# Optimization experiments

Hardware: AMD Instinct MI355X
Metric: run time of the kernel (lower is better)

The kernel has to match this reference:

```python
import jax, jax.numpy as jnp
import numpy as np

ALPHA = 6.0
BETA = 1.8
D = 256
P = 4096


def setup_inputs() -> dict:
    key = jax.random.key(0)
    k1, k2, k3 = jax.random.split(key, 3)
    pts = jax.random.normal(k1, (1, 16384, 3), dtype=jnp.float32)
    # strict_standard_normal is a shuffled Gaussian quantile grid; a standard
    # normal draw is statistically equivalent for a correctness baseline.
    A = jax.random.normal(k2, (3, D), dtype=jnp.float32) * ALPHA
    B = jax.random.normal(k3, (3, P), dtype=jnp.float32) * BETA
    return {"pts": pts, "A": A, "B": B}


def reference(pts, A, B):
    d = A.shape[-1]
    sqrt_d = jnp.asarray(d, jnp.float32) ** 0.5
    pA = pts @ A            # (b, n, d)
    pB = pts @ B            # (b, n, p)
    eA = jnp.concatenate([jnp.cos(pA), jnp.sin(pA)], axis=-1)  # (b, n, 2d)
    eB = jnp.concatenate([jnp.cos(pB), jnp.sin(pB)], axis=-1)  # (b, n, 2p)
    # linear-attention-style chain: eB @ (eB^T @ eA)
    T = jnp.einsum('bnp,bnd->bpd', eB, eA)   # (b, 2p, 2d)
    G = jnp.einsum('bnp,bpd->bnd', eB, T)    # (b, n, 2d)
    Gc = jax.lax.complex(G[..., :d], G[..., d:]) / jax.lax.complex(eA[..., :d], eA[..., d:])
    Gc = Gc / jnp.linalg.norm(Gc, axis=-1, keepdims=True) * sqrt_d
    return Gc
```

## Files before the change

kernel.cpp:

```cpp
#include <hip/hip_runtime.h>

#define NPTS 16384
#define DH 256
#define PH 4096
#define D2 512
#define LDA 40

typedef _Float16 f16;
typedef _Float16 f16x4 __attribute__((ext_vector_type(4)));
typedef _Float16 f16x8 __attribute__((ext_vector_type(8)));
typedef float f32x4 __attribute__((ext_vector_type(4)));

__device__ f16   g_eAt[D2][NPTS];
__device__ f16   g_Tt[8][D2][2*PH];
__device__ f16   g_Ts[D2][2*PH];
__device__ float g_G[4][NPTS][D2];

__device__ __forceinline__ void gload16(const void* g, void* l) {
    __builtin_amdgcn_global_load_lds((const __attribute__((address_space(1))) void*)g,
                                     (__attribute__((address_space(3))) void*)l, 16, 0, 0);
}

__global__ __launch_bounds__(256) void ker_pre(const float* __restrict__ pts,
                                               const float* __restrict__ A) {
    const int dd = blockIdx.x;
    const int t  = threadIdx.x;
    const float a0 = A[dd], a1 = A[DH + dd], a2 = A[2*DH + dd];
    f16* rowc = &g_eAt[dd][t*64];
    f16* rows = &g_eAt[DH + dd][t*64];
    #pragma unroll
    for (int s = 0; s < 8; ++s) {
        const int nb = t*64 + 8*s;
        f16x8 vc, vs;
        #pragma unroll
        for (int i = 0; i < 8; ++i) {
            const float* pr = pts + (size_t)(nb + i)*3;
            float sn, cs_; __sincosf(pr[0]*a0 + pr[1]*a1 + pr[2]*a2, &sn, &cs_);
            vc[i] = (f16)cs_; vs[i] = (f16)sn;
        }
        *(f16x8*)(rowc + 8*s) = vc;
        *(f16x8*)(rows + 8*s) = vs;
    }
}

__global__ __launch_bounds__(512) void ker_T(const float* __restrict__ pts,
                                             const float* __restrict__ B) {
    const int q0 = blockIdx.x * 64;
    const int d0 = blockIdx.y * 256;
    const int ks = blockIdx.z;
    const int t  = threadIdx.x;
    const int lane = t & 63, wid = t >> 6;
    const int wm = wid >> 2, wn = wid & 3;

    __shared__ f16 Al[128][LDA];
    __shared__ f16 Bl[256][32];

    f32x4 acc[4][4];
    #pragma unroll
    for (int a = 0; a < 4; ++a)
        #pragma unroll
        for (int bq = 0; bq < 4; ++bq) acc[a][bq] = (f32x4){0.f,0.f,0.f,0.f};

    const int qq  = t >> 3;
    const int nn0 = (t & 7) * 4;
    const float b0 = B[q0+qq], b1 = B[PH+q0+qq], b2 = B[2*PH+q0+qq];
    const int brow = 32*wid + (lane >> 2);
    const size_t bsrc0 = (size_t)(d0 + brow)*NPTS + 8*(lane & 3);
    const int mrow = wm*64 + (lane & 15);
    const int ncol = wn*64 + (lane & 15);
    const int kof  = (lane >> 4) * 8;

    for (int c = 0; c < 64; ++c) {
        const int nb = ks*2048 + c*32;
        __syncthreads();
        {
            const float* pbase = pts + (size_t)(nb + nn0)*3;
            const float4 P0 = *(const float4*)(pbase);
            const float4 P1 = *(const float4*)(pbase + 4);
            const float4 P2 = *(const float4*)(pbase + 8);
            const float px[4] = {P0.x, P0.w, P1.z, P2.y};
            const float py[4] = {P0.y, P1.x, P1.w, P2.z};
            const float pz[4] = {P0.z, P1.y, P2.x, P2.w};
            f16x4 vc, vs;
            #pragma unroll
            for (int u = 0; u < 4; ++u) {
                float sn, cc; __sincosf(px[u]*b0 + py[u]*b1 + pz[u]*b2, &sn, &cc);
                vc[u] = (f16)cc; vs[u] = (f16)sn;
            }
            *(f16x4*)&Al[qq][nn0]      = vc;
            *(f16x4*)&Al[64 + qq][nn0] = vs;
        }
        gload16(&g_eAt[0][0] + bsrc0 + (size_t)nb,                    &Bl[32*wid][0]);
        gload16(&g_eAt[0][0] + bsrc0 + (size_t)16*NPTS + (size_t)nb,  &Bl[32*wid + 16][0]);
        __syncthreads();
        f16x8 af[4], bf[4];
        #pragma unroll
        for (int mf = 0; mf < 4; ++mf) af[mf] = *(const f16x8*)&Al[mrow + mf*16][kof];
        #pragma unroll
        for (int nf = 0; nf < 4; ++nf) bf[nf] = *(const f16x8*)&Bl[ncol + nf*16][kof];
        #pragma unroll
        for (int mf = 0; mf < 4; ++mf)
            #pragma unroll
            for (int nf = 0; nf < 4; ++nf)
                acc[mf][nf] = __builtin_amdgcn_mfma_f32_16x16x32_f16(
                    af[mf], bf[nf], acc[mf][nf], 0, 0, 0);
    }
    #pragma unroll
    for (int mf = 0; mf < 4; ++mf) {
        const int qrow = q0 + mf*16 + (lane >> 4)*4;
        #pragma unroll
        for (int nf = 0; nf < 4; ++nf) {
            const int d = d0 + wn*64 + nf*16 + (lane & 15);
            f16x4 v;
            #pragma unroll
            for (int j = 0; j < 4; ++j) v[j] = (f16)acc[mf][nf][j];
            *(f16x4*)&g_Tt[ks][d][(size_t)wm*PH + qrow] = v;
        }
    }
}

__global__ __launch_bounds__(256) void ker_tsum() {
    const size_t i = ((size_t)blockIdx.x*256 + threadIdx.x) * 8;
    float o[8] = {0,0,0,0,0,0,0,0};
    #pragma unroll
    for (int z = 0; z < 8; ++z) {
        const f16x8 v = *(const f16x8*)(&g_Tt[z][0][0] + i);
        #pragma unroll
        for (int j = 0; j < 8; ++j) o[j] += (float)v[j];
    }
    f16x8 r;
    #pragma unroll
    for (int j = 0; j < 8; ++j) r[j] = (f16)o[j];
    *(f16x8*)(&g_Ts[0][0] + i) = r;
}

__global__ __launch_bounds__(512) void ker_G(const float* __restrict__ pts,
                                             const float* __restrict__ B) {
    const int n0 = blockIdx.x * 128;
    const int d0 = blockIdx.y * 256;
    const int ks = blockIdx.z;
    const int t  = threadIdx.x;
    const int lane = t & 63, wid = t >> 6;
    const int wm = wid >> 2, wn = wid & 3;

    __shared__ f16 Ac[128][LDA], As[128][LDA];
    __shared__ f16 Bc[256][32],  Bs[256][32];

    f32x4 acc[4][4];
    #pragma unroll
    for (int a = 0; a < 4; ++a)
        #pragma unroll
        for (int bq = 0; bq < 4; ++bq) acc[a][bq] = (f32x4){0.f,0.f,0.f,0.f};

    const int nn  = t >> 2;
    const int qq0 = (t & 3) * 8;
    const float px = pts[(size_t)(n0+nn)*3];
    const float py = pts[(size_t)(n0+nn)*3 + 1];
    const float pz = pts[(size_t)(n0+nn)*3 + 2];
    const int brow = 32*wid + (lane >> 2);
    const size_t bsrc0 = (size_t)(d0 + brow)*(2*PH) + 8*(lane & 3);
    const int mrow = wm*64 + (lane & 15);
    const int ncol = wn*64 + (lane & 15);
    const int kof  = (lane >> 4) * 8;

    for (int c = 0; c < 32; ++c) {
        const int qk = ks*1024 + c*32;
        __syncthreads();
        {
            const int qg = qk + qq0;
            const float4 bx0 = *(const float4*)&B[qg];
            const float4 bx1 = *(const float4*)&B[qg + 4];
            const float4 by0 = *(const float4*)&B[PH + qg];
            const float4 by1 = *(const float4*)&B[PH + qg + 4];
            const float4 bz0 = *(const float4*)&B[2*PH + qg];
            const float4 bz1 = *(const float4*)&B[2*PH + qg + 4];
            const float bx[8] = {bx0.x,bx0.y,bx0.z,bx0.w, bx1.x,bx1.y,bx1.z,bx1.w};
            const float by[8] = {by0.x,by0.y,by0.z,by0.w, by1.x,by1.y,by1.z,by1.w};
            const float bz[8] = {bz0.x,bz0.y,bz0.z,bz0.w, bz1.x,bz1.y,bz1.z,bz1.w};
            f16x8 vc, vs;
            #pragma unroll
            for (int u = 0; u < 8; ++u) {
                float sn, cc; __sincosf(px*bx[u] + py*by[u] + pz*bz[u], &sn, &cc);
                vc[u] = (f16)cc; vs[u] = (f16)sn;
            }
            *(f16x8*)&Ac[nn][qq0] = vc;
            *(f16x8*)&As[nn][qq0] = vs;
        }
        gload16(&g_Ts[0][0] + bsrc0 + (size_t)qk,                         &Bc[32*wid][0]);
        gload16(&g_Ts[0][0] + bsrc0 + (size_t)16*(2*PH) + (size_t)qk,     &Bc[32*wid + 16][0]);
        gload16(&g_Ts[0][0] + bsrc0 + (size_t)PH + (size_t)qk,            &Bs[32*wid][0]);
        gload16(&g_Ts[0][0] + bsrc0 + (size_t)(16*(2*PH) + PH) + (size_t)qk, &Bs[32*wid + 16][0]);
        __syncthreads();
        f16x8 a1[4], a2[4], b1[4], b2[4];
        #pragma unroll
        for (int mf = 0; mf < 4; ++mf) {
            a1[mf] = *(const f16x8*)&Ac[mrow + mf*16][kof];
            a2[mf] = *(const f16x8*)&As[mrow + mf*16][kof];
        }
        #pragma unroll
        for (int nf = 0; nf < 4; ++nf) {
            b1[nf] = *(const f16x8*)&Bc[ncol + nf*16][kof];
            b2[nf] = *(const f16x8*)&Bs[ncol + nf*16][kof];
        }
        #pragma unroll
        for (int mf = 0; mf < 4; ++mf)
            #pragma unroll
            for (int nf = 0; nf < 4; ++nf) {
                acc[mf][nf] = __builtin_amdgcn_mfma_f32_16x16x32_f16(
                    a1[mf], b1[nf], acc[mf][nf], 0, 0, 0);
                acc[mf][nf] = __builtin_amdgcn_mfma_f32_16x16x32_f16(
                    a2[mf], b2[nf], acc[mf][nf], 0, 0, 0);
            }
    }
    #pragma unroll
    for (int mf = 0; mf < 4; ++mf) {
        const int nbase = n0 + wm*64 + mf*16 + (lane >> 4)*4;
        #pragma unroll
        for (int nf = 0; nf < 4; ++nf) {
            const int d = d0 + wn*64 + nf*16 + (lane & 15);
            #pragma unroll
            for (int j = 0; j < 4; ++j)
                g_G[ks][nbase + j][d] = acc[mf][nf][j];
        }
    }
}

__global__ __launch_bounds__(256) void ker_fin(const float* __restrict__ pts,
                                               const float* __restrict__ A,
                                               float* __restrict__ out) {
    const int n = blockIdx.x;
    const int k = threadIdx.x;
    const float p0 = pts[(size_t)n*3], p1 = pts[(size_t)n*3+1], p2 = pts[(size_t)n*3+2];
    const float alp = p0*A[k] + p1*A[DH + k] + p2*A[2*DH + k];
    float sa, ca; __sincosf(alp, &sa, &ca);
    const float Gr = g_G[0][n][k]      + g_G[1][n][k]      + g_G[2][n][k]      + g_G[3][n][k];
    const float Gi = g_G[0][n][DH + k] + g_G[1][n][DH + k] + g_G[2][n][DH + k] + g_G[3][n][DH + k];
    const float Re = Gr*ca + Gi*sa;
    float nr = Gr*Gr + Gi*Gi;
    #pragma unroll
    for (int off = 32; off > 0; off >>= 1) nr += __shfl_down(nr, off, 64);
    __shared__ float wsum[4];
    if ((k & 63) == 0) wsum[k >> 6] = nr;
    __syncthreads();
    const float total = wsum[0] + wsum[1] + wsum[2] + wsum[3];
    const float scale = 16.0f * rsqrtf(total);
    out[(size_t)n*DH + k] = Re * scale;
}

extern "C" void kernel_launch(void* const* d_in, const int* in_sizes, int n_in,
                              void* d_out, int out_size, void* d_ws, size_t ws_size,
                              hipStream_t stream) {
    const float* pts = (const float*)d_in[0];
    const float* A   = (const float*)d_in[1];
    const float* B   = (const float*)d_in[2];
    float* out = (float*)d_out;
    (void)d_ws; (void)ws_size; (void)out_size;

    ker_pre <<<256, 256, 0, stream>>>(pts, A);
    ker_T   <<<dim3(64, 2, 8), 512, 0, stream>>>(pts, B);
    ker_tsum<<<2048, 256, 0, stream>>>();
    ker_G   <<<dim3(128, 2, 4), 512, 0, stream>>>(pts, B);
    ker_fin <<<16384, 256, 0, stream>>>(pts, A, out);
}
```

Measured before the change: 419.5 us.

## Enlarge GEMM tiles, XOR-swizzle LDS layouts, interleave cos/sin in T sum

Both MFMA kernels (T and G) now use 256x256 block tiles with a 64-wide K step, so each wave holds 8x4 accumulators. The global eA and Ts buffers are stored with an XOR swizzle over 8-element chunks, so direct global-to-LDS loads land pre-swizzled and fragment reads avoid bank conflicts without padding. The T-sum kernel writes cos/sin interleaved in this swizzled layout, which lets the G kernel merge its separate cos and sin buffers into one K=64 tile. The aim is more data reuse per LDS load and fewer bank conflicts, at the cost of more registers, lower occupancy and fewer blocks in the grid.

```diff
diff --git a/kernel.cpp b/kernel.cpp
--- a/kernel.cpp
+++ b/kernel.cpp
@@ -4,16 +4,15 @@
 #define DH 256
 #define PH 4096
 #define D2 512
-#define LDA 40
 
 typedef _Float16 f16;
 typedef _Float16 f16x4 __attribute__((ext_vector_type(4)));
 typedef _Float16 f16x8 __attribute__((ext_vector_type(8)));
 typedef float f32x4 __attribute__((ext_vector_type(4)));
 
-__device__ f16   g_eAt[D2][NPTS];
+__device__ f16   g_eAtS[(size_t)D2 * NPTS];
 __device__ f16   g_Tt[8][D2][2*PH];
-__device__ f16   g_Ts[D2][2*PH];
+__device__ f16   g_TsS[(size_t)D2 * 2*PH];
 __device__ float g_G[4][NPTS][D2];
 
 __device__ __forceinline__ void gload16(const void* g, void* l) {
@@ -26,11 +25,12 @@
     const int dd = blockIdx.x;
     const int t  = threadIdx.x;
     const float a0 = A[dd], a1 = A[DH + dd], a2 = A[2*DH + dd];
-    f16* rowc = &g_eAt[dd][t*64];
-    f16* rows = &g_eAt[DH + dd][t*64];
+    f16* rowc = &g_eAtS[(size_t)dd*NPTS + t*64];
+    f16* rows = &g_eAtS[(size_t)(DH + dd)*NPTS + t*64];
+    const int sx = dd & 7;
     #pragma unroll
     for (int s = 0; s < 8; ++s) {
-        const int nb = t*64 + 8*s;
+        const int nb = t*64 + 8*(s ^ sx);
         f16x8 vc, vs;
         #pragma unroll
         for (int i = 0; i < 8; ++i) {
@@ -45,68 +45,84 @@
 
 __global__ __launch_bounds__(512) void ker_T(const float* __restrict__ pts,
                                              const float* __restrict__ B) {
-    const int q0 = blockIdx.x * 64;
+    const int q0 = blockIdx.x * 128;
     const int d0 = blockIdx.y * 256;
     const int ks = blockIdx.z;
     const int t  = threadIdx.x;
     const int lane = t & 63, wid = t >> 6;
     const int wm = wid >> 2, wn = wid & 3;
-
-    __shared__ f16 Al[128][LDA];
-    __shared__ f16 Bl[256][32];
-
-    f32x4 acc[4][4];
-    #pragma unroll
-    for (int a = 0; a < 4; ++a)
+    const int l7 = lane & 7;
+
+    __shared__ f16 Al[256][64];
+    __shared__ f16 Bl[256][64];
+
+    f32x4 acc[8][4];
+    #pragma unroll
+    for (int a = 0; a < 8; ++a)
         #pragma unroll
         for (int bq = 0; bq < 4; ++bq) acc[a][bq] = (f32x4){0.f,0.f,0.f,0.f};
 
-    const int qq  = t >> 3;
-    const int nn0 = (t & 7) * 4;
+    const int qq  = t >> 2;
+    const int nch = (t & 3) * 16;
+    const int s0  = (t & 3) * 2;
+    const int sx  = qq & 7;
     const float b0 = B[q0+qq], b1 = B[PH+q0+qq], b2 = B[2*PH+q0+qq];
-    const int brow = 32*wid + (lane >> 2);
-    const size_t bsrc0 = (size_t)(d0 + brow)*NPTS + 8*(lane & 3);
-    const int mrow = wm*64 + (lane & 15);
-    const int ncol = wn*64 + (lane & 15);
-    const int kof  = (lane >> 4) * 8;
-
-    for (int c = 0; c < 64; ++c) {
-        const int nb = ks*2048 + c*32;
-        __syncthreads();
+    const size_t bsrc0 = (size_t)(d0 + 32*wid + (lane >> 3))*NPTS + 8*l7;
+    const int ar = wm*128 + (lane & 15);
+    const int br = wn*64  + (lane & 15);
+
+    for (int c = 0; c < 32; ++c) {
+        const int nb = ks*2048 + c*64;
+        __syncthreads();
+        #pragma unroll
+        for (int i = 0; i < 4; ++i)
+            gload16(&g_eAtS[0] + bsrc0 + (size_t)(8*i)*NPTS + (size_t)nb,
+                    &Bl[32*wid + 8*i][0]);
         {
-            const float* pbase = pts + (size_t)(nb + nn0)*3;
-            const float4 P0 = *(const float4*)(pbase);
-            const float4 P1 = *(const float4*)(pbase + 4);
-            const float4 P2 = *(const float4*)(pbase + 8);
-            const float px[4] = {P0.x, P0.w, P1.z, P2.y};
-            const float py[4] = {P0.y, P1.x, P1.w, P2.z};
-            const float pz[4] = {P0.z, P1.y, P2.x, P2.w};
-            f16x4 vc, vs;
-            #pragma unroll
-            for (int u = 0; u < 4; ++u) {
-                float sn, cc; __sincosf(px[u]*b0 + py[u]*b1 + pz[u]*b2, &sn, &cc);
-                vc[u] = (f16)cc; vs[u] = (f16)sn;
+            const float* pb = pts + (size_t)(nb + nch)*3;
+            f16x8 vc0, vc1, vs0, vs1;
+            #pragma unroll
+            for (int g = 0; g < 4; ++g) {
+                const float4 Pa = *(const float4*)(pb + 12*g);
+                const float4 Pb = *(const float4*)(pb + 12*g + 4);
+                const float4 Pc = *(const float4*)(pb + 12*g + 8);
+                const float xx[4] = {Pa.x, Pa.w, Pb.z, Pc.y};
+                const float yy[4] = {Pa.y, Pb.x, Pb.w, Pc.z};
+                const float zz[4] = {Pa.z, Pb.y, Pc.x, Pc.w};
+                #pragma unroll
+                for (int u = 0; u < 4; ++u) {
+                    float sn, cs_;
+                    __sincosf(xx[u]*b0 + yy[u]*b1 + zz[u]*b2, &sn, &cs_);
+                    const int idx = 4*g + u;
+                    if (idx < 8) { vc0[idx] = (f16)cs_; vs0[idx] = (f16)sn; }
+                    else         { vc1[idx-8] = (f16)cs_; vs1[idx-8] = (f16)sn; }
+                }
             }
-            *(f16x4*)&Al[qq][nn0]      = vc;
-            *(f16x4*)&Al[64 + qq][nn0] = vs;
-        }
-        gload16(&g_eAt[0][0] + bsrc0 + (size_t)nb,                    &Bl[32*wid][0]);
-        gload16(&g_eAt[0][0] + bsrc0 + (size_t)16*NPTS + (size_t)nb,  &Bl[32*wid + 16][0]);
-        __syncthreads();
-        f16x8 af[4], bf[4];
-        #pragma unroll
-        for (int mf = 0; mf < 4; ++mf) af[mf] = *(const f16x8*)&Al[mrow + mf*16][kof];
-        #pragma unroll
-        for (int nf = 0; nf < 4; ++nf) bf[nf] = *(const f16x8*)&Bl[ncol + nf*16][kof];
-        #pragma unroll
-        for (int mf = 0; mf < 4; ++mf)
+            *(f16x8*)&Al[qq][((s0  ) ^ sx)*8]       = vc0;
+            *(f16x8*)&Al[qq][((s0+1) ^ sx)*8]       = vc1;
+            *(f16x8*)&Al[128 + qq][((s0  ) ^ sx)*8] = vs0;
+            *(f16x8*)&Al[128 + qq][((s0+1) ^ sx)*8] = vs1;
+        }
+        __syncthreads();
+        #pragma unroll
+        for (int kk = 0; kk < 2; ++kk) {
+            f16x8 af[8], bf[4];
+            #pragma unroll
+            for (int mf = 0; mf < 8; ++mf)
+                af[mf] = *(const f16x8*)&Al[ar + mf*16][ ((((lane>>4) + 4*kk)) ^ l7) * 8 ];
             #pragma unroll
             for (int nf = 0; nf < 4; ++nf)
-                acc[mf][nf] = __builtin_amdgcn_mfma_f32_16x16x32_f16(
-                    af[mf], bf[nf], acc[mf][nf], 0, 0, 0);
-    }
-    #pragma unroll
-    for (int mf = 0; mf < 4; ++mf) {
+                bf[nf] = *(const f16x8*)&Bl[br + nf*16][ ((((lane>>4) + 4*kk)) ^ l7) * 8 ];
+            #pragma unroll
+            for (int mf = 0; mf < 8; ++mf)
+                #pragma unroll
+                for (int nf = 0; nf < 4; ++nf)
+                    acc[mf][nf] = __builtin_amdgcn_mfma_f32_16x16x32_f16(
+                        af[mf], bf[nf], acc[mf][nf], 0, 0, 0);
+        }
+    }
+    #pragma unroll
+    for (int mf = 0; mf < 8; ++mf) {
         const int qrow = q0 + mf*16 + (lane >> 4)*4;
         #pragma unroll
         for (int nf = 0; nf < 4; ++nf) {
@@ -120,101 +136,105 @@
 }
 
 __global__ __launch_bounds__(256) void ker_tsum() {
-    const size_t i = ((size_t)blockIdx.x*256 + threadIdx.x) * 8;
-    float o[8] = {0,0,0,0,0,0,0,0};
+    const int u  = blockIdx.x*256 + threadIdx.x;
+    const int d  = u >> 10;
+    const int jj = u & 1023;
+    const int c = jj >> 3, s = jj & 7;
+    const int klb = 64*c + 8*(s ^ (d & 7));
+    const int q0_ = klb >> 1;
+    float oc[4] = {0,0,0,0}, os[4] = {0,0,0,0};
     #pragma unroll
     for (int z = 0; z < 8; ++z) {
-        const f16x8 v = *(const f16x8*)(&g_Tt[z][0][0] + i);
-        #pragma unroll
-        for (int j = 0; j < 8; ++j) o[j] += (float)v[j];
-    }
-    f16x8 r;
-    #pragma unroll
-    for (int j = 0; j < 8; ++j) r[j] = (f16)o[j];
-    *(f16x8*)(&g_Ts[0][0] + i) = r;
+        const f16x4 a  = *(const f16x4*)&g_Tt[z][d][q0_];
+        const f16x4 bs = *(const f16x4*)&g_Tt[z][d][PH + q0_];
+        #pragma unroll
+        for (int j = 0; j < 4; ++j) { oc[j] += (float)a[j]; os[j] += (float)bs[j]; }
+    }
+    f16x8 v;
+    #pragma unroll
+    for (int j = 0; j < 4; ++j) { v[2*j] = (f16)oc[j]; v[2*j+1] = (f16)os[j]; }
+    *(f16x8*)&g_TsS[(size_t)d*(2*PH) + 64*c + 8*s] = v;
 }
 
 __global__ __launch_bounds__(512) void ker_G(const float* __restrict__ pts,
                                              const float* __restrict__ B) {
-    const int n0 = blockIdx.x * 128;
+    const int n0 = blockIdx.x * 256;
     const int d0 = blockIdx.y * 256;
     const int ks = blockIdx.z;
     const int t  = threadIdx.x;
     const int lane = t & 63, wid = t >> 6;
     const int wm = wid >> 2, wn = wid & 3;
-
-    __shared__ f16 Ac[128][LDA], As[128][LDA];
-    __shared__ f16 Bc[256][32],  Bs[256][32];
-
-    f32x4 acc[4][4];
-    #pragma unroll
-    for (int a = 0; a < 4; ++a)
+    const int l7 = lane & 7;
+
+    __shared__ f16 Al[256][64];
+    __shared__ f16 Bl[256][64];
+
+    f32x4 acc[8][4];
+    #pragma unroll
+    for (int a = 0; a < 8; ++a)
         #pragma unroll
         for (int bq = 0; bq < 4; ++bq) acc[a][bq] = (f32x4){0.f,0.f,0.f,0.f};
 
-    const int nn  = t >> 2;
-    const int qq0 = (t & 3) * 8;
+    const int nn    = t >> 1;
+    const int qch   = (t & 1) * 16;
+    const int sbase = (t & 1) * 4;
+    const int sx    = nn & 7;
     const float px = pts[(size_t)(n0+nn)*3];
     const float py = pts[(size_t)(n0+nn)*3 + 1];
     const float pz = pts[(size_t)(n0+nn)*3 + 2];
-    const int brow = 32*wid + (lane >> 2);
-    const size_t bsrc0 = (size_t)(d0 + brow)*(2*PH) + 8*(lane & 3);
-    const int mrow = wm*64 + (lane & 15);
-    const int ncol = wn*64 + (lane & 15);
-    const int kof  = (lane >> 4) * 8;
+    const size_t bsrc0 = (size_t)(d0 + 32*wid + (lane >> 3))*(2*PH) + 8*l7;
+    const int ar = wm*128 + (lane & 15);
+    const int br = wn*64  + (lane & 15);
 
     for (int c = 0; c < 32; ++c) {
         const int qk = ks*1024 + c*32;
-        __syncthreads();
+        const int kb = 2*qk;
+        __syncthreads();
+        #pragma unroll
+        for (int i = 0; i < 4; ++i)
+            gload16(&g_TsS[0] + bsrc0 + (size_t)(8*i)*(2*PH) + (size_t)kb,
+                    &Bl[32*wid + 8*i][0]);
         {
-            const int qg = qk + qq0;
-            const float4 bx0 = *(const float4*)&B[qg];
-            const float4 bx1 = *(const float4*)&B[qg + 4];
-            const float4 by0 = *(const float4*)&B[PH + qg];
-            const float4 by1 = *(const float4*)&B[PH + qg + 4];
-            const float4 bz0 = *(const float4*)&B[2*PH + qg];
-            const float4 bz1 = *(const float4*)&B[2*PH + qg + 4];
-            const float bx[8] = {bx0.x,bx0.y,bx0.z,bx0.w, bx1.x,bx1.y,bx1.z,bx1.w};
-            const float by[8] = {by0.x,by0.y,by0.z,by0.w, by1.x,by1.y,by1.z,by1.w};
-            const float bz[8] = {bz0.x,bz0.y,bz0.z,bz0.w, bz1.x,bz1.y,bz1.z,bz1.w};
-            f16x8 vc, vs;
-            #pragma unroll
-            for (int u = 0; u < 8; ++u) {
-                float sn, cc; __sincosf(px*bx[u] + py*by[u] + pz*bz[u], &sn, &cc);
-                vc[u] = (f16)cc; vs[u] = (f16)sn;
+            const int qg = qk + qch;
+            #pragma unroll
+            for (int g = 0; g < 4; ++g) {
+                const float4 X = *(const float4*)&B[qg + 4*g];
+                const float4 Y = *(const float4*)&B[PH + qg + 4*g];
+                const float4 Z = *(const float4*)&B[2*PH + qg + 4*g];
+                const float bx[4] = {X.x, X.y, X.z, X.w};
+                const float by[4] = {Y.x, Y.y, Y.z, Y.w};
+                const float bz[4] = {Z.x, Z.y, Z.z, Z.w};
+                f16x8 vv;
+                #pragma unroll
+                for (int u = 0; u < 4; ++u) {
+                    float sn, cs_;
+                    __sincosf(px*bx[u] + py*by[u] + pz*bz[u], &sn, &cs_);
+                    vv[2*u] = (f16)cs_; vv[2*u+1] = (f16)sn;
+                }
+                *(f16x8*)&Al[nn][((sbase + g) ^ sx)*8] = vv;
             }
-            *(f16x8*)&Ac[nn][qq0] = vc;
-            *(f16x8*)&As[nn][qq0] = vs;
-        }
-        gload16(&g_Ts[0][0] + bsrc0 + (size_t)qk,                         &Bc[32*wid][0]);
-        gload16(&g_Ts[0][0] + bsrc0 + (size_t)16*(2*PH) + (size_t)qk,     &Bc[32*wid + 16][0]);
-        gload16(&g_Ts[0][0] + bsrc0 + (size_t)PH + (size_t)qk,            &Bs[32*wid][0]);
-        gload16(&g_Ts[0][0] + bsrc0 + (size_t)(16*(2*PH) + PH) + (size_t)qk, &Bs[32*wid + 16][0]);
-        __syncthreads();
-        f16x8 a1[4], a2[4], b1[4], b2[4];
-        #pragma unroll
-        for (int mf = 0; mf < 4; ++mf) {
-            a1[mf] = *(const f16x8*)&Ac[mrow + mf*16][kof];
-            a2[mf] = *(const f16x8*)&As[mrow + mf*16][kof];
-        }
-        #pragma unroll
-        for (int nf = 0; nf < 4; ++nf) {
-            b1[nf] = *(const f16x8*)&Bc[ncol + nf*16][kof];
-            b2[nf] = *(const f16x8*)&Bs[ncol + nf*16][kof];
-        }
-        #pragma unroll
-        for (int mf = 0; mf < 4; ++mf)
-            #pragma unroll
-            for (int nf = 0; nf < 4; ++nf) {
-                acc[mf][nf] = __builtin_amdgcn_mfma_f32_16x16x32_f16(
-                    a1[mf], b1[nf], acc[mf][nf], 0, 0, 0);
-                acc[mf][nf] = __builtin_amdgcn_mfma_f32_16x16x32_f16(
-                    a2[mf], b2[nf], acc[mf][nf], 0, 0, 0);
-            }
-    }
-    #pragma unroll
-    for (int mf = 0; mf < 4; ++mf) {
-        const int nbase = n0 + wm*64 + mf*16 + (lane >> 4)*4;
+        }
+        __syncthreads();
+        #pragma unroll
+        for (int kk = 0; kk < 2; ++kk) {
+            f16x8 af[8], bf[4];
+            #pragma unroll
+            for (int mf = 0; mf < 8; ++mf)
+                af[mf] = *(const f16x8*)&Al[ar + mf*16][ ((((lane>>4) + 4*kk)) ^ l7) * 8 ];
+            #pragma unroll
+            for (int nf = 0; nf < 4; ++nf)
+                bf[nf] = *(const f16x8*)&Bl[br + nf*16][ ((((lane>>4) + 4*kk)) ^ l7) * 8 ];
+            #pragma unroll
+            for (int mf = 0; mf < 8; ++mf)
+                #pragma unroll
+                for (int nf = 0; nf < 4; ++nf)
+                    acc[mf][nf] = __builtin_amdgcn_mfma_f32_16x16x32_f16(
+                        af[mf], bf[nf], acc[mf][nf], 0, 0, 0);
+        }
+    }
+    #pragma unroll
+    for (int mf = 0; mf < 8; ++mf) {
+        const int nbase = n0 + wm*128 + mf*16 + (lane >> 4)*4;
         #pragma unroll
         for (int nf = 0; nf < 4; ++nf) {
             const int d = d0 + wn*64 + nf*16 + (lane & 15);
@@ -257,8 +277,8 @@
     (void)d_ws; (void)ws_size; (void)out_size;
 
     ker_pre <<<256, 256, 0, stream>>>(pts, A);
-    ker_T   <<<dim3(64, 2, 8), 512, 0, stream>>>(pts, B);
+    ker_T   <<<dim3(32, 2, 8), 512, 0, stream>>>(pts, B);
     ker_tsum<<<2048, 256, 0, stream>>>();
-    ker_G   <<<dim3(128, 2, 4), 512, 0, stream>>>(pts, B);
+    ker_G   <<<dim3(64, 2, 4), 512, 0, stream>>>(pts, B);
     ker_fin <<<16384, 256, 0, stream>>>(pts, A, out);
 }
```

New measurement: 491.2 us. 1.17x slower.
